# Kernel tuning notes

Measured on AMD Instinct MI355X. Metric: run time of the kernel, lower is better.

## Reference

```python
import jax, jax.numpy as jnp
import numpy as np

B, N, K_OUT, NBASIS, NGLOBALS, H = 16, 2048, 128, 4, 2, 256
DIN = 1 + NBASIS + N + NGLOBALS  # norm + basis projections + all-pairs dots + globals
NEG_SLOPE = 0.01  # torch LeakyReLU default


def setup_inputs() -> dict:
    key = jax.random.key(0)
    ks = jax.random.split(key, 6)
    x = jax.random.uniform(ks[0], (B, N, 3), jnp.float32)      # positions -> dots >= 0
    u = jax.random.normal(ks[1], (B, NGLOBALS), jnp.float32)
    basis = jax.random.normal(ks[2], (B, NBASIS, 3), jnp.float32)
    def init_w(k, fan_in, fan_out):
        return jax.random.normal(k, (fan_in, fan_out), jnp.float32) / np.float32(np.sqrt(fan_in))
    W1 = init_w(ks[3], DIN, H); b1 = jnp.zeros((H,), jnp.float32)
    W2 = init_w(ks[4], H, H);   b2 = jnp.zeros((H,), jnp.float32)
    W3 = init_w(ks[5], H, K_OUT); b3 = jnp.zeros((K_OUT,), jnp.float32)
    return {"x": x, "u": u, "basis": basis,
            "W1": W1, "b1": b1, "W2": W2, "b2": b2, "W3": W3, "b3": b3}


def reference(x, u, basis, W1, b1, W2, b2, W3, b3):
    # per-vector norms: [B, N, 1]
    norms = jnp.linalg.norm(x, axis=-1, keepdims=True)
    # projections onto basis vectors: [B, N, NBASIS]
    proj = jnp.einsum('bid,bnd->bin', x, basis)
    # all-pairs sqrt of dot products: [B, N, N]
    dots = jnp.sqrt(jnp.einsum('bid,bjd->bij', x, x))
    # concat order matches original: globals first, then [norm, proj, dots]
    u_rep = jnp.broadcast_to(u[:, None, :], (B, N, NGLOBALS))
    scalars = jnp.concatenate([u_rep, norms, proj, dots], axis=-1)  # [B, N, DIN]
    # MLP (Linear -> LeakyReLU -> Linear -> LeakyReLU -> Linear)
    h = jax.nn.leaky_relu(scalars @ W1 + b1, NEG_SLOPE)
    h = jax.nn.leaky_relu(h @ W2 + b2, NEG_SLOPE)
    fk = h @ W3 + b3  # [B, N, K_OUT]
    # outer product with x followed by mean over input vecs, fused into one einsum
    # (avoids materializing the [B, N, K_OUT, 3] tensor)
    return jnp.einsum('bio,bid->bod', fk, x) / np.float32(N)  # [B, K_OUT, 3]
```

## Files before the change

kernel.cpp:

```cpp
#include <hip/hip_runtime.h>

typedef unsigned short u16;
typedef unsigned int   u32;

typedef __attribute__((ext_vector_type(8))) short short8;
typedef __attribute__((ext_vector_type(4))) float floatx4;
typedef __attribute__((ext_vector_type(2))) float v2f;

__device__ __forceinline__ u16 f2bf(float f) {
    u32 u = __float_as_uint(f);
    u = u + 0x7fffu + ((u >> 16) & 1u);
    return (u16)(u >> 16);
}

__device__ __forceinline__ u32 pack2bf(float s0, float s1) {
    u32 a = __float_as_uint(s0) + 0x8000u;
    u32 b = __float_as_uint(s1) + 0x8000u;
    return __builtin_amdgcn_perm(b, a, 0x07060302u);
}

__device__ __forceinline__ floatx4 mfma16(short8 a, short8 b, floatx4 c) {
    return __builtin_amdgcn_mfma_f32_16x16x32_bf16(a, b, c, 0, 0, 0);
}

__global__ void k_prep(const float* __restrict__ W1, const float* __restrict__ W2,
                       const float* __restrict__ W3, u16* __restrict__ W1frag,
                       u16* __restrict__ W2frag, u16* __restrict__ W3frag) {
    int idx = blockIdx.x * 256 + threadIdx.x;
    if (idx < 524288) {
        int kt = idx >> 13, r = idx & 8191;
        int t = r >> 4, j = (r >> 3) & 1, ji = r & 7;
        int lane = t & 63, w = t >> 6, lr = lane & 15, lq = lane >> 4;
        W1frag[idx] = f2bf(W1[(7 + kt * 32 + lq * 8 + ji) * 256 + w * 32 + j * 16 + lr]);
    } else if (idx < 589824) {
        int i = idx - 524288;
        int kt = i >> 13, r = i & 8191;
        int t = r >> 5, jj = (r >> 3) & 3, ji = r & 7;
        int lane = t & 63, wv = t >> 6, lr = lane & 15, lq = lane >> 4;
        W2frag[i] = f2bf(W2[(kt * 32 + lq * 8 + ji) * 256 + wv * 64 + jj * 16 + lr]);
    } else if (idx < 622592) {
        int i = idx - 589824;
        int kt = i >> 12, r = i & 4095;
        int t = r >> 4, j = (r >> 3) & 1, ji = r & 7;
        int lane = t & 63, wv = t >> 6, lr = lane & 15, lq = lane >> 4;
        W3frag[i] = f2bf(W3[(kt * 32 + lq * 8 + ji) * 128 + wv * 32 + j * 16 + lr]);
    }
}

__global__ __launch_bounds__(512, 4) void k_h1(
    const float* __restrict__ x, const float* __restrict__ u,
    const float* __restrict__ basis, const float* __restrict__ W1,
    const float* __restrict__ b1, const u16* __restrict__ W1frag,
    u16* __restrict__ h1) {
    __shared__ float xls[6144];
    __shared__ u16 As[2][64][40];
    __shared__ float rowsml[64][6];
    __shared__ float colsml[256][6];

    const int t = threadIdx.x;
    const int b = blockIdx.y;
    const int i0 = blockIdx.x * 64;
    const int lane = t & 63, w = t >> 6;
    const int lr = lane & 15, lq = lane >> 4;

    {
        const float4* src = (const float4*)(x + b * 6144);
#pragma unroll
        for (int kk = 0; kk < 3; ++kk) {
            int q = t + kk * 512;
            float4 v = src[q];
            float vv[4] = {v.x, v.y, v.z, v.w};
            int e = q * 4;
#pragma unroll
            for (int cc = 0; cc < 4; ++cc) {
                int ee = e + cc;
                xls[(ee % 3) * 2048 + ee / 3] = vv[cc];
            }
        }
    }
    if (t < 256) {
        int c = t;
        float u0 = u[b * 2 + 0], u1 = u[b * 2 + 1];
        colsml[c][0] = b1[c] + u0 * W1[c] + u1 * W1[256 + c];
        colsml[c][1] = W1[512 + c];
        colsml[c][2] = W1[768 + c];
        colsml[c][3] = W1[1024 + c];
        colsml[c][4] = W1[1280 + c];
        colsml[c][5] = W1[1536 + c];
    }
    __syncthreads();
    if (t < 64) {
        float xx = xls[i0 + t], xy = xls[2048 + i0 + t], xz = xls[4096 + i0 + t];
        rowsml[t][0] = sqrtf(xx * xx + xy * xy + xz * xz);
#pragma unroll
        for (int p = 0; p < 4; ++p) {
            const float* bp = basis + (b * 4 + p) * 3;
            rowsml[t][1 + p] = xx * bp[0] + xy * bp[1] + xz * bp[2];
        }
    }
    const float ax = xls[i0 + lane];
    const float ay = xls[2048 + i0 + lane];
    const float az = xls[4096 + i0 + lane];
    const u16* wf = W1frag + t * 16;
    const float4* X4 = (const float4*)xls;

    auto gen_store = [&](int kt, int buf) {
        int q = kt * 8 + w;
        float4 xv = X4[q], yv = X4[512 + q], zv = X4[1024 + q];
        v2f xlo = {xv.x, xv.y}, xhi = {xv.z, xv.w};
        v2f ylo = {yv.x, yv.y}, yhi = {yv.z, yv.w};
        v2f zlo = {zv.x, zv.y}, zhi = {zv.z, zv.w};
        v2f dlo = xlo * ax, dhi = xhi * ax;
        dlo += ylo * ay; dhi += yhi * ay;
        dlo += zlo * az; dhi += zhi * az;
        float s0 = __builtin_amdgcn_sqrtf(dlo.x);
        float s1 = __builtin_amdgcn_sqrtf(dlo.y);
        float s2 = __builtin_amdgcn_sqrtf(dhi.x);
        float s3 = __builtin_amdgcn_sqrtf(dhi.y);
        uint2 dv; dv.x = pack2bf(s0, s1); dv.y = pack2bf(s2, s3);
        *(uint2*)&As[buf][lane][w * 4] = dv;
    };

    floatx4 acc[4][2];
    const floatx4 zero = {0.f, 0.f, 0.f, 0.f};
#pragma unroll
    for (int i = 0; i < 4; ++i)
#pragma unroll
        for (int j = 0; j < 2; ++j) acc[i][j] = zero;

    short8 acur[4], bcur[2], bnxt[2];
    gen_store(0, 0);
#pragma unroll
    for (int j = 0; j < 2; ++j) bcur[j] = *(const short8*)(wf + j * 8);
    __syncthreads();
#pragma unroll
    for (int i = 0; i < 4; ++i) acur[i] = *(const short8*)&As[0][i * 16 + lr][lq * 8];

#pragma unroll 2
    for (int kt = 0; kt < 64; ++kt) {
        if (kt < 63) {
            const u16* wn = wf + (kt + 1) * 8192;
#pragma unroll
            for (int j = 0; j < 2; ++j) bnxt[j] = *(const short8*)(wn + j * 8);
            gen_store(kt + 1, (kt + 1) & 1);
        }
#pragma unroll
        for (int i = 0; i < 4; ++i)
#pragma unroll
            for (int j = 0; j < 2; ++j)
                acc[i][j] = mfma16(acur[i], bcur[j], acc[i][j]);
        __syncthreads();
        if (kt < 63) {
#pragma unroll
            for (int i = 0; i < 4; ++i)
                acur[i] = *(const short8*)&As[(kt + 1) & 1][i * 16 + lr][lq * 8];
#pragma unroll
            for (int j = 0; j < 2; ++j) bcur[j] = bnxt[j];
        }
    }

    const int c0 = w * 32 + lr, c1 = c0 + 16;
    float c0v[6], c1v[6];
#pragma unroll
    for (int q = 0; q < 6; ++q) { c0v[q] = colsml[c0][q]; c1v[q] = colsml[c1][q]; }
#pragma unroll
    for (int i = 0; i < 4; ++i) {
#pragma unroll
        for (int r = 0; r < 4; ++r) {
            int row = i * 16 + lq * 4 + r;
            float nrm = rowsml[row][0];
            float p0 = rowsml[row][1], p1 = rowsml[row][2];
            float p2 = rowsml[row][3], p3 = rowsml[row][4];
            u16* orow = h1 + (b * 2048 + i0 + row) * 256;
            float v0 = acc[i][0][r] + c0v[0] + nrm * c0v[1] +
                       p0 * c0v[2] + p1 * c0v[3] + p2 * c0v[4] + p3 * c0v[5];
            v0 = v0 > 0.f ? v0 : 0.01f * v0;
            orow[c0] = f2bf(v0);
            float v1 = acc[i][1][r] + c1v[0] + nrm * c1v[1] +
                       p0 * c1v[2] + p1 * c1v[3] + p2 * c1v[4] + p3 * c1v[5];
            v1 = v1 > 0.f ? v1 : 0.01f * v1;
            orow[c1] = f2bf(v1);
        }
    }
}

__global__ __launch_bounds__(256, 2) void k_tail(
    const u16* __restrict__ h1, const u16* __restrict__ W2frag,
    const float* __restrict__ b2, const u16* __restrict__ W3frag,
    const float* __restrict__ b3, const float* __restrict__ x,
    float* __restrict__ accum) {
    __shared__ u16 h2s[64][264];
    __shared__ float colb2[256];
    __shared__ float colb3[128];
    __shared__ float xs[64][4];
    __shared__ float red[128][4];

    const int t = threadIdx.x;
    const int m0 = blockIdx.x * 64;
    const int b = m0 >> 11, i0 = m0 & 2047;
    const int lane = t & 63, wv = t >> 6;
    const int lr = lane & 15, lq = lane >> 4;

    colb2[t] = b2[t];
    if (t < 128) colb3[t] = b3[t];
    if (t < 64) {
        const float* xp = x + (b * 2048 + i0 + t) * 3;
        xs[t][0] = xp[0]; xs[t][1] = xp[1]; xs[t][2] = xp[2];
    }

    floatx4 acc[4][4];
    const floatx4 zero = {0.f, 0.f, 0.f, 0.f};
#pragma unroll
    for (int i = 0; i < 4; ++i)
#pragma unroll
        for (int j = 0; j < 4; ++j) acc[i][j] = zero;

    const u16* hsrc = h1 + m0 * 256 + lr * 256 + lq * 8;
    const u16* w2s = W2frag + t * 32;
#pragma unroll 2
    for (int kt = 0; kt < 8; ++kt) {
        short8 af[4], bf[4];
#pragma unroll
        for (int i = 0; i < 4; ++i)
            af[i] = *(const short8*)(hsrc + i * 4096 + kt * 32);
#pragma unroll
        for (int j = 0; j < 4; ++j)
            bf[j] = *(const short8*)(w2s + kt * 8192 + j * 8);
#pragma unroll
        for (int i = 0; i < 4; ++i)
#pragma unroll
            for (int j = 0; j < 4; ++j) acc[i][j] = mfma16(af[i], bf[j], acc[i][j]);
    }
#pragma unroll
    for (int i = 0; i < 4; ++i)
#pragma unroll
        for (int r = 0; r < 4; ++r) {
            int row = i * 16 + lq * 4 + r;
#pragma unroll
            for (int j = 0; j < 4; ++j) {
                int col = wv * 64 + j * 16 + lr;
                float v = acc[i][j][r] + colb2[col];
                v = v > 0.f ? v : 0.01f * v;
                h2s[row][col] = f2bf(v);
            }
        }
    __syncthreads();

    floatx4 acc2[4][2];
#pragma unroll
    for (int i = 0; i < 4; ++i)
#pragma unroll
        for (int j = 0; j < 2; ++j) acc2[i][j] = zero;

    const u16* w3s = W3frag + t * 16;
#pragma unroll 2
    for (int kt = 0; kt < 8; ++kt) {
        short8 af[4], bf[2];
#pragma unroll
        for (int i = 0; i < 4; ++i)
            af[i] = *(const short8*)&h2s[i * 16 + lr][kt * 32 + lq * 8];
#pragma unroll
        for (int j = 0; j < 2; ++j)
            bf[j] = *(const short8*)(w3s + kt * 4096 + j * 8);
#pragma unroll
        for (int i = 0; i < 4; ++i)
#pragma unroll
            for (int j = 0; j < 2; ++j) acc2[i][j] = mfma16(af[i], bf[j], acc2[i][j]);
    }

    float s[2][3];
#pragma unroll
    for (int j = 0; j < 2; ++j) { s[j][0] = 0.f; s[j][1] = 0.f; s[j][2] = 0.f; }
#pragma unroll
    for (int i = 0; i < 4; ++i)
#pragma unroll
        for (int r = 0; r < 4; ++r) {
            int row = i * 16 + lq * 4 + r;
            float x0 = xs[row][0], x1 = xs[row][1], x2 = xs[row][2];
#pragma unroll
            for (int j = 0; j < 2; ++j) {
                int col = wv * 32 + j * 16 + lr;
                float fk = acc2[i][j][r] + colb3[col];
                s[j][0] += fk * x0; s[j][1] += fk * x1; s[j][2] += fk * x2;
            }
        }
#pragma unroll
    for (int j = 0; j < 2; ++j)
#pragma unroll
        for (int d = 0; d < 3; ++d) {
            float v = s[j][d];
            v += __shfl_xor(v, 16);
            v += __shfl_xor(v, 32);
            if (lane < 16) red[wv * 32 + j * 16 + lane][d] = v;
        }
    __syncthreads();
    if (t < 128) {
#pragma unroll
        for (int d = 0; d < 3; ++d)
            atomicAdd(&accum[(b * 128 + t) * 3 + d], red[t][d]);
    }
}

__global__ void k_fin(const float* __restrict__ accum, float* __restrict__ out) {
    int idx = blockIdx.x * 256 + threadIdx.x;
    if (idx < 6144) out[idx] = accum[idx] * (1.0f / 2048.0f);
}

extern "C" void kernel_launch(void* const* d_in, const int* in_sizes, int n_in,
                              void* d_out, int out_size, void* d_ws, size_t ws_size,
                              hipStream_t stream) {
    const float* x     = (const float*)d_in[0];
    const float* u     = (const float*)d_in[1];
    const float* basis = (const float*)d_in[2];
    const float* W1    = (const float*)d_in[3];
    const float* b1    = (const float*)d_in[4];
    const float* W2    = (const float*)d_in[5];
    const float* b2    = (const float*)d_in[6];
    const float* W3    = (const float*)d_in[7];
    const float* b3    = (const float*)d_in[8];
    float* out = (float*)d_out;

    char* ws = (char*)d_ws;
    u16*  W1frag = (u16*)ws;
    u16*  W2frag = (u16*)(ws + 1048576);
    u16*  W3frag = (u16*)(ws + 1179648);
    u16*  h1     = (u16*)(ws + 1245184);
    float* accum = (float*)(ws + 18022400);

    hipMemsetAsync(accum, 0, 24576, stream);
    k_prep<<<2432, 256, 0, stream>>>(W1, W2, W3, W1frag, W2frag, W3frag);
    k_h1<<<dim3(32, 16), 512, 0, stream>>>(x, u, basis, W1, b1, W1frag, h1);
    k_tail<<<512, 256, 0, stream>>>(h1, W2frag, b2, W3frag, b3, x, accum);
    k_fin<<<24, 256, 0, stream>>>(accum, out);
}
```

Baseline: 143.6 us.

## Restructure W1 GEMM with split-K waves, LDS-staged weight prep, wider tiles

The weight-fragment prep kernel now uses 80 blocks, each staging a 32-row weight slab in LDS and writing fragments with vectorized stores. The old version used one thread per element with scattered reads. The h1 kernel drops the full per-batch x staging in LDS. Its eight waves now split the K loop two ways and compute 64x64 output tiles per wave, then reduce the two K halves through LDS. It also generates each sqrt-dot A fragment straight from global x, with 8 values per thread. The tail kernel raises its occupancy hint to 4, shrinks the h2s padding, and splits the A-fragment LDS reads into two 8-byte loads. The extra reduction pass and the higher register pressure from the larger accumulator tiles are the main risks.

```diff
diff --git a/kernel.cpp b/kernel.cpp
--- a/kernel.cpp
+++ b/kernel.cpp
@@ -5,7 +5,6 @@
 
 typedef __attribute__((ext_vector_type(8))) short short8;
 typedef __attribute__((ext_vector_type(4))) float floatx4;
-typedef __attribute__((ext_vector_type(2))) float v2f;
 
 __device__ __forceinline__ u16 f2bf(float f) {
     u32 u = __float_as_uint(f);
@@ -23,27 +22,67 @@
     return __builtin_amdgcn_mfma_f32_16x16x32_bf16(a, b, c, 0, 0, 0);
 }
 
-__global__ void k_prep(const float* __restrict__ W1, const float* __restrict__ W2,
-                       const float* __restrict__ W3, u16* __restrict__ W1frag,
-                       u16* __restrict__ W2frag, u16* __restrict__ W3frag) {
-    int idx = blockIdx.x * 256 + threadIdx.x;
-    if (idx < 524288) {
-        int kt = idx >> 13, r = idx & 8191;
-        int t = r >> 4, j = (r >> 3) & 1, ji = r & 7;
-        int lane = t & 63, w = t >> 6, lr = lane & 15, lq = lane >> 4;
-        W1frag[idx] = f2bf(W1[(7 + kt * 32 + lq * 8 + ji) * 256 + w * 32 + j * 16 + lr]);
-    } else if (idx < 589824) {
-        int i = idx - 524288;
-        int kt = i >> 13, r = i & 8191;
-        int t = r >> 5, jj = (r >> 3) & 3, ji = r & 7;
-        int lane = t & 63, wv = t >> 6, lr = lane & 15, lq = lane >> 4;
-        W2frag[i] = f2bf(W2[(kt * 32 + lq * 8 + ji) * 256 + wv * 64 + jj * 16 + lr]);
-    } else if (idx < 622592) {
-        int i = idx - 589824;
-        int kt = i >> 12, r = i & 4095;
-        int t = r >> 4, j = (r >> 3) & 1, ji = r & 7;
-        int lane = t & 63, wv = t >> 6, lr = lane & 15, lq = lane >> 4;
-        W3frag[i] = f2bf(W3[(kt * 32 + lq * 8 + ji) * 128 + wv * 32 + j * 16 + lr]);
+__global__ __launch_bounds__(256) void k_prep(
+    const float* __restrict__ W1, const float* __restrict__ W2,
+    const float* __restrict__ W3, u16* __restrict__ W1frag,
+    u16* __restrict__ W2frag, u16* __restrict__ W3frag) {
+    __shared__ float ws[32][257];
+    const int t = threadIdx.x;
+    const int mode = blockIdx.x;
+    const int lane = t & 63, grp = t >> 6;
+    const int lr = lane & 15, lq = lane >> 4;
+
+    if (mode < 64) {
+        const int kt = mode;
+#pragma unroll
+        for (int i = 0; i < 32; ++i) {
+            int idx2 = t + i * 256;
+            ws[idx2 >> 8][idx2 & 255] = W1[(7 + kt * 32 + (idx2 >> 8)) * 256 + (idx2 & 255)];
+        }
+        __syncthreads();
+        u16 arr[32];
+#pragma unroll
+        for (int f = 0; f < 4; ++f)
+#pragma unroll
+            for (int ji = 0; ji < 8; ++ji)
+                arr[f * 8 + ji] = f2bf(ws[lq * 8 + ji][grp * 64 + f * 16 + lr]);
+        uint4* dst = (uint4*)(W1frag + kt * 8192 + t * 32);
+#pragma unroll
+        for (int q = 0; q < 4; ++q) dst[q] = ((const uint4*)arr)[q];
+    } else if (mode < 72) {
+        const int kt = mode - 64;
+#pragma unroll
+        for (int i = 0; i < 32; ++i) {
+            int idx2 = t + i * 256;
+            ws[idx2 >> 8][idx2 & 255] = W2[(kt * 32 + (idx2 >> 8)) * 256 + (idx2 & 255)];
+        }
+        __syncthreads();
+        u16 arr[32];
+#pragma unroll
+        for (int f = 0; f < 4; ++f)
+#pragma unroll
+            for (int ji = 0; ji < 8; ++ji)
+                arr[f * 8 + ji] = f2bf(ws[lq * 8 + ji][grp * 64 + f * 16 + lr]);
+        uint4* dst = (uint4*)(W2frag + kt * 8192 + t * 32);
+#pragma unroll
+        for (int q = 0; q < 4; ++q) dst[q] = ((const uint4*)arr)[q];
+    } else {
+        const int kt = mode - 72;
+#pragma unroll
+        for (int i = 0; i < 16; ++i) {
+            int idx2 = t + i * 256;
+            ws[idx2 >> 7][idx2 & 127] = W3[(kt * 32 + (idx2 >> 7)) * 128 + (idx2 & 127)];
+        }
+        __syncthreads();
+        u16 arr[16];
+#pragma unroll
+        for (int j = 0; j < 2; ++j)
+#pragma unroll
+            for (int ji = 0; ji < 8; ++ji)
+                arr[j * 8 + ji] = f2bf(ws[lq * 8 + ji][grp * 32 + j * 16 + lr]);
+        uint4* dst = (uint4*)(W3frag + kt * 4096 + t * 16);
+        dst[0] = ((const uint4*)arr)[0];
+        dst[1] = ((const uint4*)arr)[1];
     }
 }
 
@@ -52,32 +91,18 @@
     const float* __restrict__ basis, const float* __restrict__ W1,
     const float* __restrict__ b1, const u16* __restrict__ W1frag,
     u16* __restrict__ h1) {
-    __shared__ float xls[6144];
-    __shared__ u16 As[2][64][40];
+    __shared__ u16 As[2][2][2048];
+    __shared__ floatx4 redbuf[2048];
     __shared__ float rowsml[64][6];
     __shared__ float colsml[256][6];
 
     const int t = threadIdx.x;
     const int b = blockIdx.y;
     const int i0 = blockIdx.x * 64;
-    const int lane = t & 63, w = t >> 6;
+    const int lane = t & 63, wv = t >> 6;
     const int lr = lane & 15, lq = lane >> 4;
-
-    {
-        const float4* src = (const float4*)(x + b * 6144);
-#pragma unroll
-        for (int kk = 0; kk < 3; ++kk) {
-            int q = t + kk * 512;
-            float4 v = src[q];
-            float vv[4] = {v.x, v.y, v.z, v.w};
-            int e = q * 4;
-#pragma unroll
-            for (int cc = 0; cc < 4; ++cc) {
-                int ee = e + cc;
-                xls[(ee % 3) * 2048 + ee / 3] = vv[cc];
-            }
-        }
-    }
+    const int k2 = wv & 1, n4 = wv >> 1;
+
     if (t < 256) {
         int c = t;
         float u0 = u[b * 2 + 0], u1 = u[b * 2 + 1];
@@ -88,9 +113,9 @@
         colsml[c][4] = W1[1280 + c];
         colsml[c][5] = W1[1536 + c];
     }
-    __syncthreads();
     if (t < 64) {
-        float xx = xls[i0 + t], xy = xls[2048 + i0 + t], xz = xls[4096 + i0 + t];
+        const float* xp = x + (b * 2048 + i0 + t) * 3;
+        float xx = xp[0], xy = xp[1], xz = xp[2];
         rowsml[t][0] = sqrtf(xx * xx + xy * xy + xz * xz);
 #pragma unroll
         for (int p = 0; p < 4; ++p) {
@@ -98,98 +123,114 @@
             rowsml[t][1 + p] = xx * bp[0] + xy * bp[1] + xz * bp[2];
         }
     }
-    const float ax = xls[i0 + lane];
-    const float ay = xls[2048 + i0 + lane];
-    const float az = xls[4096 + i0 + lane];
-    const u16* wf = W1frag + t * 16;
-    const float4* X4 = (const float4*)xls;
-
-    auto gen_store = [&](int kt, int buf) {
-        int q = kt * 8 + w;
-        float4 xv = X4[q], yv = X4[512 + q], zv = X4[1024 + q];
-        v2f xlo = {xv.x, xv.y}, xhi = {xv.z, xv.w};
-        v2f ylo = {yv.x, yv.y}, yhi = {yv.z, yv.w};
-        v2f zlo = {zv.x, zv.y}, zhi = {zv.z, zv.w};
-        v2f dlo = xlo * ax, dhi = xhi * ax;
-        dlo += ylo * ay; dhi += yhi * ay;
-        dlo += zlo * az; dhi += zhi * az;
-        float s0 = __builtin_amdgcn_sqrtf(dlo.x);
-        float s1 = __builtin_amdgcn_sqrtf(dlo.y);
-        float s2 = __builtin_amdgcn_sqrtf(dhi.x);
-        float s3 = __builtin_amdgcn_sqrtf(dhi.y);
-        uint2 dv; dv.x = pack2bf(s0, s1); dv.y = pack2bf(s2, s3);
-        *(uint2*)&As[buf][lane][w * 4] = dv;
+
+    const int gm = t >> 8, gc = t & 255;
+    const int grow = ((gc >> 6) * 16) + (gc & 15);
+    const float* ap = x + (b * 2048 + i0 + grow) * 3;
+    const float gax = ap[0], gay = ap[1], gaz = ap[2];
+    const float* xbase = x + b * 6144;
+    const int gk = ((gc >> 4) & 3) * 8;
+
+    auto gen = [&](int ktbase, int bufsel) {
+        const float4* px = (const float4*)(xbase + ((ktbase + gm) * 32 + gk) * 3);
+        float4 p0 = px[0], p1 = px[1], p2 = px[2];
+        float s0 = __builtin_amdgcn_sqrtf(gax * p0.x + gay * p0.y + gaz * p0.z);
+        float s1 = __builtin_amdgcn_sqrtf(gax * p0.w + gay * p1.x + gaz * p1.y);
+        float s2 = __builtin_amdgcn_sqrtf(gax * p1.z + gay * p1.w + gaz * p2.x);
+        float s3 = __builtin_amdgcn_sqrtf(gax * p2.y + gay * p2.z + gaz * p2.w);
+        u32 d0 = pack2bf(s0, s1), d1 = pack2bf(s2, s3);
+        float4 p3 = px[3], p4 = px[4], p5 = px[5];
+        float s4 = __builtin_amdgcn_sqrtf(gax * p3.x + gay * p3.y + gaz * p3.z);
+        float s5 = __builtin_amdgcn_sqrtf(gax * p3.w + gay * p4.x + gaz * p4.y);
+        float s6 = __builtin_amdgcn_sqrtf(gax * p4.z + gay * p4.w + gaz * p5.x);
+        float s7 = __builtin_amdgcn_sqrtf(gax * p5.y + gay * p5.z + gaz * p5.w);
+        uint4 dv;
+        dv.x = d0; dv.y = d1;
+        dv.z = pack2bf(s4, s5); dv.w = pack2bf(s6, s7);
+        *(uint4*)&As[bufsel][gm][gc * 8] = dv;
     };
 
-    floatx4 acc[4][2];
+    floatx4 acc[4][4];
     const floatx4 zero = {0.f, 0.f, 0.f, 0.f};
 #pragma unroll
     for (int i = 0; i < 4; ++i)
 #pragma unroll
-        for (int j = 0; j < 2; ++j) acc[i][j] = zero;
-
-    short8 acur[4], bcur[2], bnxt[2];
-    gen_store(0, 0);
-#pragma unroll
-    for (int j = 0; j < 2; ++j) bcur[j] = *(const short8*)(wf + j * 8);
+        for (int f = 0; f < 4; ++f) acc[i][f] = zero;
+
+    gen(0, 0);
     __syncthreads();
-#pragma unroll
-    for (int i = 0; i < 4; ++i) acur[i] = *(const short8*)&As[0][i * 16 + lr][lq * 8];
-
-#pragma unroll 2
-    for (int kt = 0; kt < 64; ++kt) {
-        if (kt < 63) {
-            const u16* wn = wf + (kt + 1) * 8192;
-#pragma unroll
-            for (int j = 0; j < 2; ++j) bnxt[j] = *(const short8*)(wn + j * 8);
-            gen_store(kt + 1, (kt + 1) & 1);
-        }
-#pragma unroll
-        for (int i = 0; i < 4; ++i)
-#pragma unroll
-            for (int j = 0; j < 2; ++j)
-                acc[i][j] = mfma16(acur[i], bcur[j], acc[i][j]);
-        __syncthreads();
-        if (kt < 63) {
-#pragma unroll
-            for (int i = 0; i < 4; ++i)
-                acur[i] = *(const short8*)&As[(kt + 1) & 1][i * 16 + lr][lq * 8];
-#pragma unroll
-            for (int j = 0; j < 2; ++j) bcur[j] = bnxt[j];
-        }
-    }
-
-    const int c0 = w * 32 + lr, c1 = c0 + 16;
-    float c0v[6], c1v[6];
-#pragma unroll
-    for (int q = 0; q < 6; ++q) { c0v[q] = colsml[c0][q]; c1v[q] = colsml[c1][q]; }
-#pragma unroll
-    for (int i = 0; i < 4; ++i) {
-#pragma unroll
-        for (int r = 0; r < 4; ++r) {
-            int row = i * 16 + lq * 4 + r;
-            float nrm = rowsml[row][0];
-            float p0 = rowsml[row][1], p1 = rowsml[row][2];
-            float p2 = rowsml[row][3], p3 = rowsml[row][4];
-            u16* orow = h1 + (b * 2048 + i0 + row) * 256;
-            float v0 = acc[i][0][r] + c0v[0] + nrm * c0v[1] +
-                       p0 * c0v[2] + p1 * c0v[3] + p2 * c0v[4] + p3 * c0v[5];
-            v0 = v0 > 0.f ? v0 : 0.01f * v0;
-            orow[c0] = f2bf(v0);
-            float v1 = acc[i][1][r] + c1v[0] + nrm * c1v[1] +
-                       p0 * c1v[2] + p1 * c1v[3] + p2 * c1v[4] + p3 * c1v[5];
-            v1 = v1 > 0.f ? v1 : 0.01f * v1;
-            orow[c1] = f2bf(v1);
-        }
-    }
-}
-
-__global__ __launch_bounds__(256, 2) void k_tail(
+
+    for (int r = 0; r < 32; ++r) {
+        const int buf = r & 1;
+        const int kt = 2 * r + k2;
+        short8 acur[4], bcur[4];
+#pragma unroll
+        for (int i = 0; i < 4; ++i)
+            acur[i] = *(const short8*)&As[buf][k2][(i * 64 + lane) * 8];
+        const u16* bp = W1frag + ((kt * 4 + n4) * 64 + lane) * 32;
+#pragma unroll
+        for (int f = 0; f < 4; ++f) bcur[f] = *(const short8*)(bp + f * 8);
+        if (r < 31) gen(2 * r + 2, buf ^ 1);
+#pragma unroll
+        for (int i = 0; i < 4; ++i)
+#pragma unroll
+            for (int f = 0; f < 4; ++f)
+                acc[i][f] = mfma16(acur[i], bcur[f], acc[i][f]);
+        __syncthreads();
+    }
+
+#pragma unroll
+    for (int half = 0; half < 2; ++half) {
+        if (k2 == 1) {
+#pragma unroll
+            for (int iL = 0; iL < 2; ++iL)
+#pragma unroll
+                for (int f = 0; f < 4; ++f)
+                    redbuf[(n4 * 8 + iL * 4 + f) * 64 + lane] = acc[half * 2 + iL][f];
+        }
+        __syncthreads();
+        if (k2 == 0) {
+#pragma unroll
+            for (int iL = 0; iL < 2; ++iL)
+#pragma unroll
+                for (int f = 0; f < 4; ++f) {
+                    floatx4 v = redbuf[(n4 * 8 + iL * 4 + f) * 64 + lane];
+                    acc[half * 2 + iL][f] += v;
+                }
+        }
+        __syncthreads();
+    }
+
+    if (k2 == 0) {
+#pragma unroll
+        for (int i = 0; i < 4; ++i) {
+#pragma unroll
+            for (int r2 = 0; r2 < 4; ++r2) {
+                int row = i * 16 + lq * 4 + r2;
+                float nrm = rowsml[row][0];
+                float p0 = rowsml[row][1], p1 = rowsml[row][2];
+                float p2 = rowsml[row][3], p3 = rowsml[row][4];
+                u16* orow = h1 + (b * 2048 + i0 + row) * 256;
+#pragma unroll
+                for (int f = 0; f < 4; ++f) {
+                    int col = n4 * 64 + f * 16 + lr;
+                    float v = acc[i][f][r2] + colsml[col][0] + nrm * colsml[col][1] +
+                              p0 * colsml[col][2] + p1 * colsml[col][3] +
+                              p2 * colsml[col][4] + p3 * colsml[col][5];
+                    v = v > 0.f ? v : 0.01f * v;
+                    orow[col] = f2bf(v);
+                }
+            }
+        }
+    }
+}
+
+__global__ __launch_bounds__(256, 4) void k_tail(
     const u16* __restrict__ h1, const u16* __restrict__ W2frag,
     const float* __restrict__ b2, const u16* __restrict__ W3frag,
     const float* __restrict__ b3, const float* __restrict__ x,
     float* __restrict__ accum) {
-    __shared__ u16 h2s[64][264];
+    __shared__ u16 h2s[64][260];
     __shared__ float colb2[256];
     __shared__ float colb3[128];
     __shared__ float xs[64][4];
@@ -257,8 +298,12 @@
     for (int kt = 0; kt < 8; ++kt) {
         short8 af[4], bf[2];
 #pragma unroll
-        for (int i = 0; i < 4; ++i)
-            af[i] = *(const short8*)&h2s[i * 16 + lr][kt * 32 + lq * 8];
+        for (int i = 0; i < 4; ++i) {
+            union { short8 s; uint2 u2[2]; } afu;
+            afu.u2[0] = *(const uint2*)&h2s[i * 16 + lr][kt * 32 + lq * 8];
+            afu.u2[1] = *(const uint2*)&h2s[i * 16 + lr][kt * 32 + lq * 8 + 4];
+            af[i] = afu.s;
+        }
 #pragma unroll
         for (int j = 0; j < 2; ++j)
             bf[j] = *(const short8*)(w3s + kt * 4096 + j * 8);
@@ -328,7 +373,7 @@
     float* accum = (float*)(ws + 18022400);
 
     hipMemsetAsync(accum, 0, 24576, stream);
-    k_prep<<<2432, 256, 0, stream>>>(W1, W2, W3, W1frag, W2frag, W3frag);
+    k_prep<<<80, 256, 0, stream>>>(W1, W2, W3, W1frag, W2frag, W3frag);
     k_h1<<<dim3(32, 16), 512, 0, stream>>>(x, u, basis, W1, b1, W1frag, h1);
     k_tail<<<512, 256, 0, stream>>>(h1, W2frag, b2, W3frag, b3, x, accum);
     k_fin<<<24, 256, 0, stream>>>(accum, out);
```

Result: slower. 168.7 us (+17.5%).
